# Optimization experiments

Measured on AMD Instinct MI355X. Metric: run time of the kernel, lower is better.

## Reference

```python
import jax, jax.numpy as jnp
import numpy as np
import math

N = 16
ZIGZAG = np.array([135, 150, 165, 180, 195, 210, 225, 240, 241, 226, 211, 196, 181, 166, 151, 136, 121, 106, 91, 76, 61, 46, 31, 47, 62, 77, 92, 107, 122, 137, 152, 167, 182, 197, 212, 227, 242, 243, 228, 213, 198, 183, 168, 153, 138, 123, 108, 93, 78, 63, 79, 94, 109, 124, 139, 154, 169, 184, 199, 214, 229, 244, 245, 230, 215, 200, 185, 170, 155, 140, 125, 110, 95, 111, 126, 141, 156, 171, 186, 201, 216, 231, 246, 247, 232, 217, 202, 187, 172, 157, 142, 127, 143, 158, 173, 188, 203, 218, 233, 248, 249, 234, 219, 204, 189, 174, 159, 175, 190, 205, 220, 235, 250, 251, 236, 221, 206, 191, 207, 222, 237, 252, 253, 238, 223, 239, 254, 255], dtype=np.int32)

# DCT basis (harmonics) and normalization matrix, matching the torch helpers
_i = np.arange(N, dtype=np.float32)
HARM = np.cos((2.0 * _i[:, None] + 1.0) * (_i[None, :] * math.pi / (2.0 * N))).astype(np.float32)
_n = np.ones((N, 1), dtype=np.float32); _n[0, 0] = 1.0 / math.sqrt(2.0)
NMAT = (_n @ _n.T).astype(np.float32)
SCALE = 1.0 / math.sqrt(2.0 * N)


def setup_inputs() -> dict:
    key = jax.random.key(0)
    x = jax.random.normal(key, (8, 3, 1024, 1024), dtype=jnp.float32)
    return {"x": x}


def reference(x):
    b, c, h, w = x.shape
    # blockify: [b, c, n_blocks, 16, 16], blocks in row-major spatial order
    blocks = x.reshape(b, c, h // N, N, w // N, N).transpose(0, 1, 2, 4, 3, 5).reshape(b, c, -1, N, N)
    harm = jnp.asarray(HARM)
    nmat = jnp.asarray(NMAT)
    # block DCT: scale * n * (H^T @ block @ H)
    coeff = SCALE * nmat * (jnp.matmul(jnp.matmul(harm.T, blocks), harm))
    # zigzag upper-band gather: [b, c, n_blocks, 128]
    flat = coeff.reshape(b, c, -1, N * N)[..., jnp.asarray(ZIGZAG)]
    # adaptive threshold: zero out coefficients below per-block mean
    mean = jnp.mean(flat, axis=3, keepdims=True)
    sel = jnp.where(flat < mean, jnp.float32(0), flat)
    a = jnp.abs(sel) + 1e-12
    # L2 normalize along coefficient dim (torch F.normalize, eps=1e-12)
    norm = jnp.sqrt(jnp.sum(a * a, axis=3, keepdims=True))
    probs = a / jnp.maximum(norm, 1e-12)
    log_prob = jnp.log2(probs)
    entropy = jnp.mean(-jnp.sum(probs * log_prob, axis=3))
    return entropy
```

## Files before the change

### kernel.cpp

```cpp
#include <hip/hip_runtime.h>
#include <math.h>


constexpr double kPi = 3.14159265358979323846;

constexpr double ccos(double x) {
    while (x > kPi) x -= 2.0 * kPi;
    while (x < -kPi) x += 2.0 * kPi;
    double x2 = x * x;
    double term = 1.0, sum = 1.0;
    for (int k = 1; k <= 24; ++k) {
        term *= -x2 / (double)((2 * k - 1) * (2 * k));
        sum += term;
    }
    return sum;
}

struct DctTables {
    float g1[16][16];
    float g2[16][16];
    constexpr DctTables() : g1{}, g2{} {
        for (int j = 0; j < 16; ++j) {
            for (int f = 0; f < 16; ++f) {
                float colf = (float)((double)f * kPi) / 32.0f;
                float arg = (2.0f * (float)j + 1.0f) * colf;
                float h = (float)ccos((double)arg);
                float n = (f == 0) ? 0.70710678118654752440f : 1.0f;
                g1[j][f] = h * n;
                g2[j][f] = h * n * 0.17677669529663688110f;
            }
        }
    }
};
constexpr DctTables kT;

#define XS_PITCH 260
#define CZ_PITCH 136
#define NWG 6144

__global__ __launch_bounds__(256, 4) void dct_entropy_kernel(
    const float* __restrict__ x, float* __restrict__ partials) {
    __shared__ float smem[8336];
    float* Xs = smem;
    float* Ts = smem + 4160;
    float* Czz = smem;
    float* part = smem + 8320;

    const int t = threadIdx.x;
    const int g = blockIdx.x;
    const int bc = g >> 8;
    const int br = (g >> 2) & 63;
    const int cg = g & 3;
    const float* base =
        x + ((size_t)bc << 20) + ((size_t)br << 14) + ((size_t)cg << 8);

#pragma unroll
    for (int k = 0; k < 4; ++k) {
        int idx = t + 256 * k;
        int row = idx >> 6;
        int c4 = idx & 63;
        float4 ld = *(const float4*)(base + (size_t)row * 1024 + c4 * 4);
        *(float4*)(&Xs[row * XS_PITCH + c4 * 4]) = ld;
    }
    __syncthreads();

    {
        const int b = t >> 4;
        const int i = t & 15;
        float xr[16];
        const float* src = &Xs[i * XS_PITCH + b * 16];
#pragma unroll
        for (int c = 0; c < 4; ++c) {
            float4 ld = *(const float4*)(src + 4 * c);
            xr[4 * c + 0] = ld.x;
            xr[4 * c + 1] = ld.y;
            xr[4 * c + 2] = ld.z;
            xr[4 * c + 3] = ld.w;
        }
#pragma unroll
        for (int v = 0; v < 16; ++v) {
            float acc = 0.0f;
#pragma unroll
            for (int j = 0; j < 16; ++j) acc = fmaf(xr[j], kT.g1[j][v], acc);
            Ts[v * XS_PITCH + b * 16 + i] = acc;
        }
    }
    __syncthreads();

    {
        const int b = t >> 4;
        const int v = t & 15;
        float ti[16];
        const float* src = &Ts[v * XS_PITCH + b * 16];
#pragma unroll
        for (int c = 0; c < 4; ++c) {
            float4 ld = *(const float4*)(src + 4 * c);
            ti[4 * c + 0] = ld.x;
            ti[4 * c + 1] = ld.y;
            ti[4 * c + 2] = ld.z;
            ti[4 * c + 3] = ld.w;
        }
        const int hi = (v > 7) ? 1 : 0;
        const int u_min = 15 - v + hi;
        const int off = hi ? (v * (v - 1) / 2 + 8) : (v * (v + 1) / 2);
        float* wbase = &Czz[b * CZ_PITCH + off - u_min];
#pragma unroll
        for (int u = 0; u < 16; ++u) {
            float acc = 0.0f;
#pragma unroll
            for (int i = 0; i < 16; ++i) acc = fmaf(ti[i], kT.g2[i][u], acc);
            if (u >= u_min) wbase[u] = acc;
        }
    }
    __syncthreads();

    {
        const int q = t >> 4;
        const int l = t & 15;
        const float* C = &Czz[q * CZ_PITCH + 8 * l];
        float4 f0 = *(const float4*)C;
        float4 f1 = *(const float4*)(C + 4);
        float c[8] = {f0.x, f0.y, f0.z, f0.w, f1.x, f1.y, f1.z, f1.w};

        float s = ((c[0] + c[1]) + (c[2] + c[3])) +
                  ((c[4] + c[5]) + (c[6] + c[7]));
#pragma unroll
        for (int m = 1; m <= 8; m <<= 1) s += __shfl_xor(s, m);
        const float mean = s * (1.0f / 128.0f);

        float a[8];
        float sq = 0.0f;
#pragma unroll
        for (int j = 0; j < 8; ++j) {
            a[j] = (c[j] < mean) ? 1e-12f : (fabsf(c[j]) + 1e-12f);
            sq = fmaf(a[j], a[j], sq);
        }
#pragma unroll
        for (int m = 1; m <= 8; m <<= 1) sq += __shfl_xor(sq, m);
        const float inv = 1.0f / fmaxf(sqrtf(sq), 1e-12f);

        float e = 0.0f;
#pragma unroll
        for (int j = 0; j < 8; ++j) {
            float p = a[j] * inv;
            e = fmaf(p, __log2f(p), e);
        }
#pragma unroll
        for (int m = 1; m <= 8; m <<= 1) e += __shfl_xor(e, m);
        if (l == 0) part[q] = e;
    }
    __syncthreads();

    if (t == 0) {
        float tot = 0.0f;
#pragma unroll
        for (int i = 0; i < 16; ++i) tot += part[i];
        partials[g] = tot;
    }
}

__global__ __launch_bounds__(256) void reduce_partials(
    const float* __restrict__ partials, float* __restrict__ out) {
    __shared__ float s[4];
    float v = 0.0f;
    for (int i = threadIdx.x; i < NWG; i += 256) v += partials[i];
#pragma unroll
    for (int off = 32; off > 0; off >>= 1) v += __shfl_down(v, off);
    if ((threadIdx.x & 63) == 0) s[threadIdx.x >> 6] = v;
    __syncthreads();
    if (threadIdx.x == 0) {
        float tot = (s[0] + s[1]) + (s[2] + s[3]);
        out[0] = tot * (-1.0f / 98304.0f);
    }
}

extern "C" void kernel_launch(void* const* d_in, const int* in_sizes, int n_in,
                              void* d_out, int out_size, void* d_ws,
                              size_t ws_size, hipStream_t stream) {
    const float* x = (const float*)d_in[0];
    float* out = (float*)d_out;
    float* ws = (float*)d_ws;
    dct_entropy_kernel<<<NWG, 256, 0, stream>>>(x, ws);
    reduce_partials<<<1, 256, 0, stream>>>(ws, out);
}
```

Baseline: 147.4 us.

## Make each wave own one block-strip, replacing block barriers with wave-local LDS fences

Each wave now loads its 4 DCT blocks directly from global memory into registers, skipping the shared-memory staging pass. Transposes go through a per-wave 1K-float LDS region with an XOR swizzle instead of padded pitches, and __syncthreads is replaced by s_waitcnt lgkmcnt(0) fences. LDS use drops to 16KB per workgroup, which allows 8 workgroups per CU, and partials are written per wave and reduced by a wider 1024-thread final kernel. The risks are direct global loads that are less coalesced (16 rows of 64B per wave) and relying on wave-synchronous LDS ordering.

```diff
diff --git a/kernel.cpp b/kernel.cpp
--- a/kernel.cpp
+++ b/kernel.cpp
@@ -34,90 +34,86 @@
 };
 constexpr DctTables kT;
 
-#define XS_PITCH 260
-#define CZ_PITCH 136
 #define NWG 6144
+#define NPART (NWG * 4)
 
-__global__ __launch_bounds__(256, 4) void dct_entropy_kernel(
+#define WAVE_LDS_FENCE() asm volatile("s_waitcnt lgkmcnt(0)" ::: "memory")
+
+__global__ __launch_bounds__(256, 8) void dct_entropy_kernel(
     const float* __restrict__ x, float* __restrict__ partials) {
-    __shared__ float smem[8336];
-    float* Xs = smem;
-    float* Ts = smem + 4160;
-    float* Czz = smem;
-    float* part = smem + 8320;
+    __shared__ float smem[4096];
 
     const int t = threadIdx.x;
+    const int wave = t >> 6;
+    const int lane = t & 63;
+    const int b = lane >> 4;
+    const int il = lane & 15;
+    float* R = smem + (wave << 10);
+
     const int g = blockIdx.x;
     const int bc = g >> 8;
     const int br = (g >> 2) & 63;
     const int cg = g & 3;
-    const float* base =
-        x + ((size_t)bc << 20) + ((size_t)br << 14) + ((size_t)cg << 8);
+    const float* base = x + ((size_t)bc << 20) + ((size_t)br << 14) +
+                        (cg << 8) + (wave << 6) + (b << 4);
 
-#pragma unroll
-    for (int k = 0; k < 4; ++k) {
-        int idx = t + 256 * k;
-        int row = idx >> 6;
-        int c4 = idx & 63;
-        float4 ld = *(const float4*)(base + (size_t)row * 1024 + c4 * 4);
-        *(float4*)(&Xs[row * XS_PITCH + c4 * 4]) = ld;
-    }
-    __syncthreads();
-
+    float xr[16];
     {
-        const int b = t >> 4;
-        const int i = t & 15;
-        float xr[16];
-        const float* src = &Xs[i * XS_PITCH + b * 16];
+        const float* gp = base + (size_t)il * 1024;
 #pragma unroll
         for (int c = 0; c < 4; ++c) {
-            float4 ld = *(const float4*)(src + 4 * c);
+            float4 ld = *(const float4*)(gp + 4 * c);
             xr[4 * c + 0] = ld.x;
             xr[4 * c + 1] = ld.y;
             xr[4 * c + 2] = ld.z;
             xr[4 * c + 3] = ld.w;
         }
+    }
+    {
+        const int cc = (b << 2) + (il >> 2);
+        const int lo = il & 3;
 #pragma unroll
         for (int v = 0; v < 16; ++v) {
             float acc = 0.0f;
 #pragma unroll
             for (int j = 0; j < 16; ++j) acc = fmaf(xr[j], kT.g1[j][v], acc);
-            Ts[v * XS_PITCH + b * 16 + i] = acc;
+            R[(v << 6) + ((cc ^ v) << 2) + lo] = acc;
         }
     }
-    __syncthreads();
+    WAVE_LDS_FENCE();
 
+    float ti[16];
     {
-        const int b = t >> 4;
-        const int v = t & 15;
-        float ti[16];
-        const float* src = &Ts[v * XS_PITCH + b * 16];
 #pragma unroll
         for (int c = 0; c < 4; ++c) {
-            float4 ld = *(const float4*)(src + 4 * c);
+            const int ch = (b << 2) + c;
+            float4 ld = *(const float4*)(&R[(il << 6) + ((ch ^ il) << 2)]);
             ti[4 * c + 0] = ld.x;
             ti[4 * c + 1] = ld.y;
             ti[4 * c + 2] = ld.z;
             ti[4 * c + 3] = ld.w;
         }
+    }
+    WAVE_LDS_FENCE();
+    {
+        const int v = il;
         const int hi = (v > 7) ? 1 : 0;
         const int u_min = 15 - v + hi;
         const int off = hi ? (v * (v - 1) / 2 + 8) : (v * (v + 1) / 2);
-        float* wbase = &Czz[b * CZ_PITCH + off - u_min];
+        float* wb = &R[b * 136 + off - u_min];
 #pragma unroll
         for (int u = 0; u < 16; ++u) {
             float acc = 0.0f;
 #pragma unroll
             for (int i = 0; i < 16; ++i) acc = fmaf(ti[i], kT.g2[i][u], acc);
-            if (u >= u_min) wbase[u] = acc;
+            if (u >= u_min) wb[u] = acc;
         }
     }
-    __syncthreads();
+    WAVE_LDS_FENCE();
 
     {
-        const int q = t >> 4;
-        const int l = t & 15;
-        const float* C = &Czz[q * CZ_PITCH + 8 * l];
+        const int q = lane >> 4;
+        const float* C = &R[q * 136 + ((lane & 15) << 3)];
         float4 f0 = *(const float4*)C;
         float4 f1 = *(const float4*)(C + 4);
         float c[8] = {f0.x, f0.y, f0.z, f0.w, f1.x, f1.y, f1.z, f1.w};
@@ -146,31 +142,29 @@
             e = fmaf(p, __log2f(p), e);
         }
 #pragma unroll
-        for (int m = 1; m <= 8; m <<= 1) e += __shfl_xor(e, m);
-        if (l == 0) part[q] = e;
-    }
-    __syncthreads();
-
-    if (t == 0) {
-        float tot = 0.0f;
-#pragma unroll
-        for (int i = 0; i < 16; ++i) tot += part[i];
-        partials[g] = tot;
+        for (int m = 1; m <= 32; m <<= 1) e += __shfl_xor(e, m);
+        if (lane == 0) partials[(g << 2) + wave] = e;
     }
 }
 
-__global__ __launch_bounds__(256) void reduce_partials(
+__global__ __launch_bounds__(1024) void reduce_partials(
     const float* __restrict__ partials, float* __restrict__ out) {
-    __shared__ float s[4];
+    __shared__ float s[16];
     float v = 0.0f;
-    for (int i = threadIdx.x; i < NWG; i += 256) v += partials[i];
+    const float4* p4 = (const float4*)partials;
+    for (int i = threadIdx.x; i < NPART / 4; i += 1024) {
+        float4 f = p4[i];
+        v += (f.x + f.y) + (f.z + f.w);
+    }
 #pragma unroll
-    for (int off = 32; off > 0; off >>= 1) v += __shfl_down(v, off);
+    for (int m = 1; m <= 32; m <<= 1) v += __shfl_xor(v, m);
     if ((threadIdx.x & 63) == 0) s[threadIdx.x >> 6] = v;
     __syncthreads();
-    if (threadIdx.x == 0) {
-        float tot = (s[0] + s[1]) + (s[2] + s[3]);
-        out[0] = tot * (-1.0f / 98304.0f);
+    if (threadIdx.x < 16) {
+        float tot = s[threadIdx.x];
+#pragma unroll
+        for (int m = 1; m <= 8; m <<= 1) tot += __shfl_xor(tot, m);
+        if (threadIdx.x == 0) out[0] = tot * (-1.0f / 98304.0f);
     }
 }
 
@@ -181,5 +175,5 @@
     float* out = (float*)d_out;
     float* ws = (float*)d_ws;
     dct_entropy_kernel<<<NWG, 256, 0, stream>>>(x, ws);
-    reduce_partials<<<1, 256, 0, stream>>>(ws, out);
+    reduce_partials<<<1, 1024, 0, stream>>>(ws, out);
 }
```

New measurement: 144.6 us. About the same (-1.9%).
